# Kernel tuning notes

Hardware: AMD Instinct MI355X
Metric: run time of the kernel (lower is better)

Reference implementation:

```python
import jax, jax.numpy as jnp
import numpy as np

B, V, J, P = 1024, 5023, 5, 36
PARENTS = np.array([0, 0, 1, 1, 1], dtype=np.int64)  # FLAME kinematic chain


def setup_inputs() -> dict:
    key = jax.random.key(0)
    ks = jax.random.split(key, 8)
    return {
        "v_shaped_expressed": jax.random.normal(ks[0], (B, V, 3), jnp.float32) * 0.1,
        "global_pose_params_6d": jax.random.normal(ks[1], (B, 6), jnp.float32),
        "neck_pose_params_ax": jax.random.normal(ks[2], (B, 3), jnp.float32) * 0.1,
        "jaw_pose_params_ax": jax.random.normal(ks[3], (B, 3), jnp.float32) * 0.1,
        "eye_pose_params_ax": jax.random.normal(ks[4], (B, 6), jnp.float32) * 0.1,
        "J_transformed_rest": jax.random.normal(ks[5], (B, J, 3), jnp.float32) * 0.1,
        "lbs_weights": jax.nn.softmax(jax.random.normal(ks[6], (V, J), jnp.float32), axis=-1),
        "posedirs": jax.random.normal(ks[7], (V, P, 3), jnp.float32) * 0.01,
        "parents": jnp.asarray(PARENTS),
    }


def batch_rodrigues(rv, eps=1e-8):
    # rv: [B,3] axis-angle -> [B,3,3] rotation matrices
    angle = jnp.linalg.norm(rv + eps, axis=1, keepdims=True)  # [B,1]
    d = rv / angle
    cos = jnp.cos(angle)[:, :, None]
    sin = jnp.sin(angle)[:, :, None]
    rx, ry, rz = d[:, 0], d[:, 1], d[:, 2]
    z = jnp.zeros_like(rx)
    K = jnp.stack([z, -rz, ry, rz, z, -rx, -ry, rx, z], axis=1).reshape(-1, 3, 3)
    I = jnp.eye(3, dtype=rv.dtype)[None]
    return I + sin * K + (1.0 - cos) * (K @ K)


def rot6d_to_matrix(x):
    # Zhou et al. 6D rotation -> [B,3,3] (rows b1,b2,b3, as pytorch3d)
    a1, a2 = x[:, :3], x[:, 3:]
    b1 = a1 / jnp.linalg.norm(a1, axis=-1, keepdims=True)
    b2 = a2 - jnp.sum(b1 * a2, axis=-1, keepdims=True) * b1
    b2 = b2 / jnp.linalg.norm(b2, axis=-1, keepdims=True)
    b3 = jnp.cross(b1, b2)
    return jnp.stack([b1, b2, b3], axis=-2)


def make_T(R, t):
    # R [...,3,3], t [...,3] -> homogeneous [...,4,4]
    top = jnp.concatenate([R, t[..., None]], axis=-1)
    bot = jnp.broadcast_to(jnp.array([0.0, 0.0, 0.0, 1.0], R.dtype), top.shape[:-2] + (1, 4))
    return jnp.concatenate([top, bot], axis=-2)


def batch_rigid_transform(rot_mats, joints, parents):
    # rot_mats [B,J,3,3], joints [B,J,3]; parents: numpy int array (constant)
    rel = joints.at[:, 1:].add(-joints[:, parents[1:]])
    Tm = make_T(rot_mats, rel)  # [B,J,4,4]
    chain = [Tm[:, 0]]
    for i in range(1, parents.shape[0]):  # tiny fixed chain (J=5)
        chain.append(chain[int(parents[i])] @ Tm[:, i])
    tr = jnp.stack(chain, axis=1)  # [B,J,4,4]
    posed_joints = tr[:, :, :3, 3]
    R = tr[:, :, :3, :3]
    t = posed_joints - jnp.einsum('bjhw,bjw->bjh', R, joints)
    return posed_joints, make_T(R, t)


def reference(v_shaped_expressed, global_pose_params_6d, neck_pose_params_ax,
              jaw_pose_params_ax, eye_pose_params_ax, J_transformed_rest,
              lbs_weights, posedirs, parents):
    parents = np.asarray(parents)
    Rg = rot6d_to_matrix(global_pose_params_6d)
    Rn = batch_rodrigues(neck_pose_params_ax)
    Rj = batch_rodrigues(jaw_pose_params_ax)
    Rel = batch_rodrigues(eye_pose_params_ax[:, :3])
    Rer = batch_rodrigues(eye_pose_params_ax[:, 3:])
    rot_mats = jnp.stack([Rg, Rn, Rj, Rel, Rer], axis=1)  # [B,5,3,3]

    _, A = batch_rigid_transform(rot_mats, J_transformed_rest, parents)  # [B,5,4,4]

    # pose blendshapes from joints 1..4 (neck/jaw/eyes): [B, 36]
    b = rot_mats.shape[0]
    pose_feat = (rot_mats[:, 1:5] - jnp.eye(3, dtype=rot_mats.dtype)).reshape(b, -1)
    pose_bs = jnp.einsum('bp,vpc->bvc', pose_feat, posedirs)
    v = v_shaped_expressed + pose_bs  # [B,V,3]

    # linear blend skinning
    T = jnp.einsum('vj,bjhw->bvhw', lbs_weights, A)  # [B,V,4,4]
    v_h = jnp.concatenate([v, jnp.ones(v.shape[:2] + (1,), v.dtype)], axis=-1)
    v_posed = jnp.einsum('bvhw,bvw->bvh', T, v_h)[:, :, :3]
    return v_posed
```

## Files before the change

### kernel.cpp

```cpp
#include <hip/hip_runtime.h>
#include <math.h>

constexpr int Bn = 1024, Vn = 5023;
constexpr int NB = 32;
constexpr int PARAM_STRIDE = 96;


__device__ inline void rodrigues3(float rx, float ry, float rz, float R[9]) {
    const float eps = 1e-8f;
    float ax = rx + eps, ay = ry + eps, az = rz + eps;
    float ang = sqrtf(ax * ax + ay * ay + az * az);
    float inv = 1.0f / ang;
    float dx = rx * inv, dy = ry * inv, dz = rz * inv;
    float s = sinf(ang), c = cosf(ang), omc = 1.0f - c;
    float K[9] = {0.f, -dz, dy, dz, 0.f, -dx, -dy, dx, 0.f};
    float K2[9];
#pragma unroll
    for (int r = 0; r < 3; r++)
#pragma unroll
        for (int k = 0; k < 3; k++) {
            float acc = 0.f;
#pragma unroll
            for (int i = 0; i < 3; i++) acc += K[r * 3 + i] * K[i * 3 + k];
            K2[r * 3 + k] = acc;
        }
#pragma unroll
    for (int i = 0; i < 9; i++) R[i] = s * K[i] + omc * K2[i];
    R[0] += 1.f; R[4] += 1.f; R[8] += 1.f;
}

__device__ inline void rot6d(const float* x, float R[9]) {
    float a1x = x[0], a1y = x[1], a1z = x[2];
    float a2x = x[3], a2y = x[4], a2z = x[5];
    float n1 = sqrtf(a1x * a1x + a1y * a1y + a1z * a1z);
    float b1x = a1x / n1, b1y = a1y / n1, b1z = a1z / n1;
    float d = b1x * a2x + b1y * a2y + b1z * a2z;
    float tx = a2x - d * b1x, ty = a2y - d * b1y, tz = a2z - d * b1z;
    float n2 = sqrtf(tx * tx + ty * ty + tz * tz);
    float b2x = tx / n2, b2y = ty / n2, b2z = tz / n2;
    float b3x = b1y * b2z - b1z * b2y;
    float b3y = b1z * b2x - b1x * b2z;
    float b3z = b1x * b2y - b1y * b2x;
    R[0] = b1x; R[1] = b1y; R[2] = b1z;
    R[3] = b2x; R[4] = b2y; R[5] = b2z;
    R[6] = b3x; R[7] = b3y; R[8] = b3z;
}

__device__ inline void compose(const float* Rp, const float* tp,
                               const float* Ri, const float* ti,
                               float* Ro, float* to) {
#pragma unroll
    for (int r = 0; r < 3; r++) {
#pragma unroll
        for (int c = 0; c < 3; c++) {
            Ro[r * 3 + c] = Rp[r * 3 + 0] * Ri[0 * 3 + c] +
                            Rp[r * 3 + 1] * Ri[1 * 3 + c] +
                            Rp[r * 3 + 2] * Ri[2 * 3 + c];
        }
        to[r] = Rp[r * 3 + 0] * ti[0] + Rp[r * 3 + 1] * ti[1] +
                Rp[r * 3 + 2] * ti[2] + tp[r];
    }
}

__global__ void flame_params_kernel(const float* __restrict__ g6,
                                    const float* __restrict__ neck,
                                    const float* __restrict__ jaw,
                                    const float* __restrict__ eye,
                                    const float* __restrict__ jrest,
                                    float* __restrict__ params) {
    int b = blockIdx.x * blockDim.x + threadIdx.x;
    if (b >= Bn) return;

    float R[5][9];
    rot6d(g6 + b * 6, R[0]);
    rodrigues3(neck[b * 3 + 0], neck[b * 3 + 1], neck[b * 3 + 2], R[1]);
    rodrigues3(jaw[b * 3 + 0], jaw[b * 3 + 1], jaw[b * 3 + 2], R[2]);
    rodrigues3(eye[b * 6 + 0], eye[b * 6 + 1], eye[b * 6 + 2], R[3]);
    rodrigues3(eye[b * 6 + 3], eye[b * 6 + 4], eye[b * 6 + 5], R[4]);

    float j[5][3];
#pragma unroll
    for (int i = 0; i < 5; i++) {
        j[i][0] = jrest[b * 15 + i * 3 + 0];
        j[i][1] = jrest[b * 15 + i * 3 + 1];
        j[i][2] = jrest[b * 15 + i * 3 + 2];
    }
    float rel[5][3];
#pragma unroll
    for (int c = 0; c < 3; c++) {
        rel[0][c] = j[0][c];
        rel[1][c] = j[1][c] - j[0][c];
        rel[2][c] = j[2][c] - j[1][c];
        rel[3][c] = j[3][c] - j[1][c];
        rel[4][c] = j[4][c] - j[1][c];
    }

    float CR[5][9], CT[5][3];
#pragma unroll
    for (int i = 0; i < 9; i++) CR[0][i] = R[0][i];
#pragma unroll
    for (int c = 0; c < 3; c++) CT[0][c] = rel[0][c];
    compose(CR[0], CT[0], R[1], rel[1], CR[1], CT[1]);
    compose(CR[1], CT[1], R[2], rel[2], CR[2], CT[2]);
    compose(CR[1], CT[1], R[3], rel[3], CR[3], CT[3]);
    compose(CR[1], CT[1], R[4], rel[4], CR[4], CT[4]);

    float* P = params + b * PARAM_STRIDE;
#pragma unroll
    for (int jj = 0; jj < 4; jj++)
#pragma unroll
        for (int r = 0; r < 3; r++)
#pragma unroll
            for (int c = 0; c < 3; c++)
                P[jj * 9 + r * 3 + c] = R[jj + 1][r * 3 + c] - (r == c ? 1.f : 0.f);
#pragma unroll
    for (int i = 0; i < 5; i++) {
#pragma unroll
        for (int r = 0; r < 3; r++) {
            float t = CT[i][r] - (CR[i][r * 3 + 0] * j[i][0] +
                                  CR[i][r * 3 + 1] * j[i][1] +
                                  CR[i][r * 3 + 2] * j[i][2]);
            P[36 + i * 12 + r * 4 + 0] = CR[i][r * 3 + 0];
            P[36 + i * 12 + r * 4 + 1] = CR[i][r * 3 + 1];
            P[36 + i * 12 + r * 4 + 2] = CR[i][r * 3 + 2];
            P[36 + i * 12 + r * 4 + 3] = t;
        }
    }
}

__global__ __launch_bounds__(256) void flame_main_kernel(
    const float* __restrict__ vsh, const float* __restrict__ lbs,
    const float* __restrict__ pdirs, const float* __restrict__ params,
    float* __restrict__ out) {
    int v = blockIdx.x * 256 + threadIdx.x;
    bool valid = v < Vn;
    int vc = valid ? v : (Vn - 1);

    float pd[108];
#pragma unroll
    for (int i = 0; i < 27; i++) {
        float4 t = *reinterpret_cast<const float4*>(pdirs + (size_t)vc * 108 + i * 4);
        pd[i * 4 + 0] = t.x;
        pd[i * 4 + 1] = t.y;
        pd[i * 4 + 2] = t.z;
        pd[i * 4 + 3] = t.w;
    }
    float w[5];
#pragma unroll
    for (int jj = 0; jj < 5; jj++) w[jj] = lbs[(size_t)vc * 5 + jj];

    int b0 = blockIdx.y * NB;
    for (int bi = 0; bi < NB; bi++) {
        int b = b0 + bi;
        const float* __restrict__ P = params + b * PARAM_STRIDE;

        float ax = 0.f, ay = 0.f, az = 0.f;
#pragma unroll
        for (int p = 0; p < 36; p++) {
            float f = P[p];
            ax = fmaf(f, pd[p * 3 + 0], ax);
            ay = fmaf(f, pd[p * 3 + 1], ay);
            az = fmaf(f, pd[p * 3 + 2], az);
        }

        size_t base = ((size_t)b * Vn + vc) * 3;
        float x = vsh[base + 0] + ax;
        float y = vsh[base + 1] + ay;
        float z = vsh[base + 2] + az;

        float ox = 0.f, oy = 0.f, oz = 0.f;
#pragma unroll
        for (int jj = 0; jj < 5; jj++) {
            const float* Aj = P + 36 + jj * 12;
            float wj = w[jj];
            float rx = fmaf(Aj[0], x, fmaf(Aj[1], y, fmaf(Aj[2], z, Aj[3])));
            float ry = fmaf(Aj[4], x, fmaf(Aj[5], y, fmaf(Aj[6], z, Aj[7])));
            float rz = fmaf(Aj[8], x, fmaf(Aj[9], y, fmaf(Aj[10], z, Aj[11])));
            ox = fmaf(wj, rx, ox);
            oy = fmaf(wj, ry, oy);
            oz = fmaf(wj, rz, oz);
        }
        if (valid) {
            out[base + 0] = ox;
            out[base + 1] = oy;
            out[base + 2] = oz;
        }
    }
}

extern "C" void kernel_launch(void* const* d_in, const int* in_sizes, int n_in,
                              void* d_out, int out_size, void* d_ws, size_t ws_size,
                              hipStream_t stream) {
    const float* vsh   = (const float*)d_in[0];
    const float* g6    = (const float*)d_in[1];
    const float* neck  = (const float*)d_in[2];
    const float* jaw   = (const float*)d_in[3];
    const float* eye   = (const float*)d_in[4];
    const float* jrest = (const float*)d_in[5];
    const float* lbs   = (const float*)d_in[6];
    const float* pdirs = (const float*)d_in[7];
    float* out = (float*)d_out;
    float* params = (float*)d_ws;

    hipLaunchKernelGGL(flame_params_kernel, dim3((Bn + 255) / 256), dim3(256), 0,
                       stream, g6, neck, jaw, eye, jrest, params);

    dim3 grid((Vn + 255) / 256, Bn / NB);
    hipLaunchKernelGGL(flame_main_kernel, grid, dim3(256), 0, stream, vsh, lbs,
                       pdirs, params, out);
}
```

Baseline: 59.47 us.

## Stream posedirs in chunks and keep per-batch accumulators in registers

Instead of holding all 108 posedirs values per vertex in registers, the kernel loads them in 12-float chunks with a one-step software prefetch and applies each chunk to 8 batch accumulators. NB drops from 32 to 8, so the grid has more blocks along the batch axis and each block needs fewer registers, aiming at higher occupancy. The trade-off is that posedirs are reloaded by four times as many blocks, and param loads are spread through the loop.

```diff
diff --git a/kernel.cpp b/kernel.cpp
--- a/kernel.cpp
+++ b/kernel.cpp
@@ -2,7 +2,7 @@
 #include <math.h>
 
 constexpr int Bn = 1024, Vn = 5023;
-constexpr int NB = 32;
+constexpr int NB = 8;
 constexpr int PARAM_STRIDE = 96;
 
 
@@ -135,43 +135,59 @@
     int v = blockIdx.x * 256 + threadIdx.x;
     bool valid = v < Vn;
     int vc = valid ? v : (Vn - 1);
-
-    float pd[108];
-#pragma unroll
-    for (int i = 0; i < 27; i++) {
-        float4 t = *reinterpret_cast<const float4*>(pdirs + (size_t)vc * 108 + i * 4);
-        pd[i * 4 + 0] = t.x;
-        pd[i * 4 + 1] = t.y;
-        pd[i * 4 + 2] = t.z;
-        pd[i * 4 + 3] = t.w;
-    }
+    int b0 = blockIdx.y * NB;
+
+    float ax[NB], ay[NB], az[NB];
+#pragma unroll
+    for (int bi = 0; bi < NB; bi++) {
+        size_t base = ((size_t)(b0 + bi) * Vn + vc) * 3;
+        ax[bi] = vsh[base + 0];
+        ay[bi] = vsh[base + 1];
+        az[bi] = vsh[base + 2];
+    }
+
     float w[5];
 #pragma unroll
     for (int jj = 0; jj < 5; jj++) w[jj] = lbs[(size_t)vc * 5 + jj];
 
-    int b0 = blockIdx.y * NB;
+    const float* __restrict__ pv = pdirs + (size_t)vc * 108;
+    float4 c0 = *reinterpret_cast<const float4*>(pv + 0);
+    float4 c1 = *reinterpret_cast<const float4*>(pv + 4);
+    float4 c2 = *reinterpret_cast<const float4*>(pv + 8);
+
+#pragma unroll 1
+    for (int g = 0; g < 9; g++) {
+        float4 n0 = c0, n1 = c1, n2 = c2;
+        if (g < 8) {
+            n0 = *reinterpret_cast<const float4*>(pv + g * 12 + 12);
+            n1 = *reinterpret_cast<const float4*>(pv + g * 12 + 16);
+            n2 = *reinterpret_cast<const float4*>(pv + g * 12 + 20);
+        }
+        float pdv[12] = {c0.x, c0.y, c0.z, c0.w, c1.x, c1.y,
+                         c1.z, c1.w, c2.x, c2.y, c2.z, c2.w};
+#pragma unroll
+        for (int bi = 0; bi < NB; bi++) {
+            const float* __restrict__ P =
+                params + (b0 + bi) * PARAM_STRIDE + g * 4;
+#pragma unroll
+            for (int k = 0; k < 4; k++) {
+                float f = P[k];
+                ax[bi] = fmaf(f, pdv[k * 3 + 0], ax[bi]);
+                ay[bi] = fmaf(f, pdv[k * 3 + 1], ay[bi]);
+                az[bi] = fmaf(f, pdv[k * 3 + 2], az[bi]);
+            }
+        }
+        c0 = n0; c1 = n1; c2 = n2;
+    }
+
+#pragma unroll
     for (int bi = 0; bi < NB; bi++) {
-        int b = b0 + bi;
-        const float* __restrict__ P = params + b * PARAM_STRIDE;
-
-        float ax = 0.f, ay = 0.f, az = 0.f;
-#pragma unroll
-        for (int p = 0; p < 36; p++) {
-            float f = P[p];
-            ax = fmaf(f, pd[p * 3 + 0], ax);
-            ay = fmaf(f, pd[p * 3 + 1], ay);
-            az = fmaf(f, pd[p * 3 + 2], az);
-        }
-
-        size_t base = ((size_t)b * Vn + vc) * 3;
-        float x = vsh[base + 0] + ax;
-        float y = vsh[base + 1] + ay;
-        float z = vsh[base + 2] + az;
-
+        const float* __restrict__ A = params + (b0 + bi) * PARAM_STRIDE + 36;
+        float x = ax[bi], y = ay[bi], z = az[bi];
         float ox = 0.f, oy = 0.f, oz = 0.f;
 #pragma unroll
         for (int jj = 0; jj < 5; jj++) {
-            const float* Aj = P + 36 + jj * 12;
+            const float* Aj = A + jj * 12;
             float wj = w[jj];
             float rx = fmaf(Aj[0], x, fmaf(Aj[1], y, fmaf(Aj[2], z, Aj[3])));
             float ry = fmaf(Aj[4], x, fmaf(Aj[5], y, fmaf(Aj[6], z, Aj[7])));
@@ -181,6 +197,7 @@
             oz = fmaf(wj, rz, oz);
         }
         if (valid) {
+            size_t base = ((size_t)(b0 + bi) * Vn + vc) * 3;
             out[base + 0] = ox;
             out[base + 1] = oy;
             out[base + 2] = oz;
```

Result: slower. 61.26 us (+3.0%).

## Stage posedirs in LDS as packed bf16 and halve batch tile per block

Applied to the files above, without the earlier changes.

Posedirs for the block's 256 vertices are loaded with coalesced float4 reads, rounded to bf16, packed two per dword and stored in shared memory, so each thread no longer keeps 108 floats in registers. Per batch iteration the thread reads part of its row from LDS and keeps the rest in registers. Params are now read as float4, the loop is left un-unrolled, launch bounds ask for two blocks per SM, and NB drops to 16 to give more blocks. The aim is lower register pressure, better occupancy and coalesced loads, at the cost of bf16 rounding error in the pose blendshapes and about 60 KB of LDS per block.

```diff
diff --git a/kernel.cpp b/kernel.cpp
--- a/kernel.cpp
+++ b/kernel.cpp
@@ -2,8 +2,9 @@
 #include <math.h>
 
 constexpr int Bn = 1024, Vn = 5023;
-constexpr int NB = 32;
+constexpr int NB = 16;
 constexpr int PARAM_STRIDE = 96;
+constexpr int ROW_DW = 60;
 
 
 __device__ inline void rodrigues3(float rx, float ry, float rz, float R[9]) {
@@ -128,54 +129,109 @@
     }
 }
 
-__global__ __launch_bounds__(256) void flame_main_kernel(
+
+__device__ inline uint32_t pack_bf2(float a, float b) {
+    uint32_t ua = __float_as_uint(a);
+    uint32_t ub = __float_as_uint(b);
+    uint32_t ra = (ua + 0x7FFFu + ((ua >> 16) & 1u)) >> 16;
+    uint32_t rb = (ub + 0x7FFFu + ((ub >> 16) & 1u)) >> 16;
+    return (ra & 0xFFFFu) | (rb << 16);
+}
+
+#define GETD(i)                                                      \
+    (((i) & 3) == 0 ? C[(i) >> 2].x                                  \
+     : ((i) & 3) == 1 ? C[(i) >> 2].y                                \
+     : ((i) & 3) == 2 ? C[(i) >> 2].z : C[(i) >> 2].w)
+#define ACC(c) ((c) == 0 ? a0 : (c) == 1 ? a1 : a2)
+
+__global__ __launch_bounds__(256, 2) void flame_main_kernel(
     const float* __restrict__ vsh, const float* __restrict__ lbs,
     const float* __restrict__ pdirs, const float* __restrict__ params,
     float* __restrict__ out) {
-    int v = blockIdx.x * 256 + threadIdx.x;
+    int tid = threadIdx.x;
+    int v = blockIdx.x * 256 + tid;
     bool valid = v < Vn;
     int vc = valid ? v : (Vn - 1);
-
-    float pd[108];
-#pragma unroll
-    for (int i = 0; i < 27; i++) {
-        float4 t = *reinterpret_cast<const float4*>(pdirs + (size_t)vc * 108 + i * 4);
-        pd[i * 4 + 0] = t.x;
-        pd[i * 4 + 1] = t.y;
-        pd[i * 4 + 2] = t.z;
-        pd[i * 4 + 3] = t.w;
-    }
-    float w[5];
-#pragma unroll
-    for (int jj = 0; jj < 5; jj++) w[jj] = lbs[(size_t)vc * 5 + jj];
-
     int b0 = blockIdx.y * NB;
+
+    __shared__ uint32_t shd[256 * ROW_DW];
+
+    {
+        const size_t blk_base = (size_t)blockIdx.x * 256 * 108;
+        const size_t max_base = (size_t)Vn * 108 - 4;
+#pragma unroll
+        for (int c = 0; c < 27; c++) {
+            int q = c * 256 + tid;
+            size_t src = blk_base + (size_t)q * 4;
+            if (src > max_base) src = max_base;
+            float4 f = *reinterpret_cast<const float4*>(pdirs + src);
+            uint32_t d0 = pack_bf2(f.x, f.y);
+            uint32_t d1 = pack_bf2(f.z, f.w);
+            int p = q * 2;
+            int r = p / 54;
+            int k = p - r * 54;
+            shd[r * ROW_DW + k] = d0;
+            shd[r * ROW_DW + k + 1] = d1;
+        }
+    }
+    __syncthreads();
+
+    float wgt[5];
+#pragma unroll
+    for (int jj = 0; jj < 5; jj++) wgt[jj] = lbs[(size_t)vc * 5 + jj];
+
+    const uint4* __restrict__ my =
+        reinterpret_cast<const uint4*>(shd + tid * ROW_DW);
+
+    uint4 H0 = my[8], H1 = my[9], H2 = my[10], H3 = my[11], H4 = my[12],
+          H5 = my[13];
+
+#pragma unroll 1
     for (int bi = 0; bi < NB; bi++) {
         int b = b0 + bi;
-        const float* __restrict__ P = params + b * PARAM_STRIDE;
-
-        float ax = 0.f, ay = 0.f, az = 0.f;
-#pragma unroll
-        for (int p = 0; p < 36; p++) {
-            float f = P[p];
-            ax = fmaf(f, pd[p * 3 + 0], ax);
-            ay = fmaf(f, pd[p * 3 + 1], ay);
-            az = fmaf(f, pd[p * 3 + 2], az);
-        }
-
+        const float4* __restrict__ P4 =
+            reinterpret_cast<const float4*>(params + (size_t)b * PARAM_STRIDE);
         size_t base = ((size_t)b * Vn + vc) * 3;
-        float x = vsh[base + 0] + ax;
-        float y = vsh[base + 1] + ay;
-        float z = vsh[base + 2] + az;
+
+        float a0 = vsh[base + 0];
+        float a1 = vsh[base + 1];
+        float a2 = vsh[base + 2];
+
+        float fc[36];
+#pragma unroll
+        for (int g = 0; g < 9; g++) {
+            float4 f = P4[g];
+            fc[g * 4 + 0] = f.x;
+            fc[g * 4 + 1] = f.y;
+            fc[g * 4 + 2] = f.z;
+            fc[g * 4 + 3] = f.w;
+        }
+
+        uint4 C[14];
+#pragma unroll
+        for (int i = 0; i < 8; i++) C[i] = my[i];
+        C[8] = H0; C[9] = H1; C[10] = H2; C[11] = H3; C[12] = H4; C[13] = H5;
+
+#pragma unroll
+        for (int i = 0; i < 54; i++) {
+            uint32_t d = GETD(i);
+            float flo = __uint_as_float(d << 16);
+            float fhi = __uint_as_float(d & 0xFFFF0000u);
+            const int e0 = 2 * i, e1 = 2 * i + 1;
+            ACC(e0 % 3) = fmaf(fc[e0 / 3], flo, ACC(e0 % 3));
+            ACC(e1 % 3) = fmaf(fc[e1 / 3], fhi, ACC(e1 % 3));
+        }
 
         float ox = 0.f, oy = 0.f, oz = 0.f;
 #pragma unroll
         for (int jj = 0; jj < 5; jj++) {
-            const float* Aj = P + 36 + jj * 12;
-            float wj = w[jj];
-            float rx = fmaf(Aj[0], x, fmaf(Aj[1], y, fmaf(Aj[2], z, Aj[3])));
-            float ry = fmaf(Aj[4], x, fmaf(Aj[5], y, fmaf(Aj[6], z, Aj[7])));
-            float rz = fmaf(Aj[8], x, fmaf(Aj[9], y, fmaf(Aj[10], z, Aj[11])));
+            float4 r0 = P4[9 + jj * 3 + 0];
+            float4 r1 = P4[9 + jj * 3 + 1];
+            float4 r2 = P4[9 + jj * 3 + 2];
+            float wj = wgt[jj];
+            float rx = fmaf(r0.x, a0, fmaf(r0.y, a1, fmaf(r0.z, a2, r0.w)));
+            float ry = fmaf(r1.x, a0, fmaf(r1.y, a1, fmaf(r1.z, a2, r1.w)));
+            float rz = fmaf(r2.x, a0, fmaf(r2.y, a1, fmaf(r2.z, a2, r2.w)));
             ox = fmaf(wj, rx, ox);
             oy = fmaf(wj, ry, oy);
             oz = fmaf(wj, rz, oz);
```

Measured after the change: 70.13 us. 1.18x slower.

## Stage posedirs as fp16 in LDS and scalar-load per-batch params

Applied to the files above, without the earlier changes.

Each block now converts its 128 vertices' posedirs to packed fp16 in shared memory, instead of holding 108 floats per thread in registers. It splits the batch range between two half-blocks and reloads the posedirs into 27 packed registers per group of four batches. Per-batch pose features and joint transforms are fetched with inline-asm scalar loads into SGPRs. The goal is lower VGPR pressure, higher occupancy and better latency hiding for this bandwidth-bound loop, at the cost of fp16 rounding of the posedirs and reliance on fragile inline assembly. NB is halved and the grid is reshaped to match.

```diff
diff --git a/kernel.cpp b/kernel.cpp
--- a/kernel.cpp
+++ b/kernel.cpp
@@ -2,8 +2,13 @@
 #include <math.h>
 
 constexpr int Bn = 1024, Vn = 5023;
-constexpr int NB = 32;
+constexpr int NB = 16;
 constexpr int PARAM_STRIDE = 96;
+
+typedef int i32x16 __attribute__((ext_vector_type(16)));
+typedef int i32x8 __attribute__((ext_vector_type(8)));
+typedef int i32x4 __attribute__((ext_vector_type(4)));
+typedef __fp16 half2_t __attribute__((ext_vector_type(2)));
 
 
 __device__ inline void rodrigues3(float rx, float ry, float rz, float R[9]) {
@@ -128,62 +133,123 @@
     }
 }
 
-__global__ __launch_bounds__(256) void flame_main_kernel(
+
+#define FCV(k)                                                        \
+    __int_as_float((k) < 16 ? fc0[(k)]                                \
+                   : (k) < 32 ? fc1[(k) - 16] : fc2[(k) - 32])
+#define AFV(k)                                                        \
+    __int_as_float((k) < 16 ? A0[(k)]                                 \
+                   : (k) < 32 ? A1[(k) - 16]                          \
+                   : (k) < 48 ? A2[(k) - 32]                          \
+                   : (k) < 56 ? A3[(k) - 48] : A4[(k) - 56])
+#define ACCSEL(c) ((c) == 0 ? px : (c) == 1 ? py : pz)
+
+__global__ __launch_bounds__(256, 4) void flame_main_kernel(
     const float* __restrict__ vsh, const float* __restrict__ lbs,
     const float* __restrict__ pdirs, const float* __restrict__ params,
     float* __restrict__ out) {
-    int v = blockIdx.x * 256 + threadIdx.x;
-    bool valid = v < Vn;
-    int vc = valid ? v : (Vn - 1);
-
-    float pd[108];
-#pragma unroll
-    for (int i = 0; i < 27; i++) {
-        float4 t = *reinterpret_cast<const float4*>(pdirs + (size_t)vc * 108 + i * 4);
-        pd[i * 4 + 0] = t.x;
-        pd[i * 4 + 1] = t.y;
-        pd[i * 4 + 2] = t.z;
-        pd[i * 4 + 3] = t.w;
-    }
-    float w[5];
-#pragma unroll
-    for (int jj = 0; jj < 5; jj++) w[jj] = lbs[(size_t)vc * 5 + jj];
-
-    int b0 = blockIdx.y * NB;
-    for (int bi = 0; bi < NB; bi++) {
-        int b = b0 + bi;
-        const float* __restrict__ P = params + b * PARAM_STRIDE;
-
-        float ax = 0.f, ay = 0.f, az = 0.f;
-#pragma unroll
-        for (int p = 0; p < 36; p++) {
-            float f = P[p];
-            ax = fmaf(f, pd[p * 3 + 0], ax);
-            ay = fmaf(f, pd[p * 3 + 1], ay);
-            az = fmaf(f, pd[p * 3 + 2], az);
-        }
-
-        size_t base = ((size_t)b * Vn + vc) * 3;
-        float x = vsh[base + 0] + ax;
-        float y = vsh[base + 1] + ay;
-        float z = vsh[base + 2] + az;
-
-        float ox = 0.f, oy = 0.f, oz = 0.f;
-#pragma unroll
-        for (int jj = 0; jj < 5; jj++) {
-            const float* Aj = P + 36 + jj * 12;
-            float wj = w[jj];
-            float rx = fmaf(Aj[0], x, fmaf(Aj[1], y, fmaf(Aj[2], z, Aj[3])));
-            float ry = fmaf(Aj[4], x, fmaf(Aj[5], y, fmaf(Aj[6], z, Aj[7])));
-            float rz = fmaf(Aj[8], x, fmaf(Aj[9], y, fmaf(Aj[10], z, Aj[11])));
-            ox = fmaf(wj, rx, ox);
-            oy = fmaf(wj, ry, oy);
-            oz = fmaf(wj, rz, oz);
-        }
-        if (valid) {
-            out[base + 0] = ox;
-            out[base + 1] = oy;
-            out[base + 2] = oz;
+    const int tid = threadIdx.x;
+    const int vt = tid & 127;
+    const int bh = __builtin_amdgcn_readfirstlane(tid >> 7);
+    const int v = blockIdx.x * 128 + vt;
+    const bool valid = v < Vn;
+    const int vc = valid ? v : (Vn - 1);
+    const int b0 = blockIdx.y * NB + bh * (NB / 2);
+
+    __shared__ uint32_t shd[128 * 54];
+
+    {
+        const size_t g0 = (size_t)blockIdx.x * 128 * 108;
+        const size_t gmax = (size_t)Vn * 108 - 2;
+#pragma unroll
+        for (int i = 0; i < 27; i++) {
+            int p = i * 256 + tid;
+            size_t g = g0 + (size_t)p * 2;
+            if (g > gmax) g = gmax;
+            float2 f = *reinterpret_cast<const float2*>(pdirs + g);
+            half2_t h;
+            h.x = (__fp16)f.x;
+            h.y = (__fp16)f.y;
+            shd[p] = __builtin_bit_cast(uint32_t, h);
+        }
+    }
+    __syncthreads();
+
+    float wgt[5];
+#pragma unroll
+    for (int jj = 0; jj < 5; jj++) wgt[jj] = lbs[(size_t)vc * 5 + jj];
+
+    const uint2* __restrict__ my =
+        reinterpret_cast<const uint2*>(shd + vt * 54);
+
+#pragma unroll 1
+    for (int g2 = 0; g2 < 2; g2++) {
+        uint2 C[27];
+#pragma unroll
+        for (int i = 0; i < 27; i++) C[i] = my[i];
+
+#pragma unroll
+        for (int u = 0; u < 4; u++) {
+            const int b = b0 + g2 * 4 + u;
+            const float* P = params + (size_t)b * PARAM_STRIDE;
+            const size_t base = ((size_t)b * Vn + vc) * 3;
+
+            float a0 = vsh[base + 0];
+            float a1 = vsh[base + 1];
+            float a2 = vsh[base + 2];
+
+            i32x16 fc0, fc1;
+            i32x4 fc2;
+            asm volatile("s_load_dwordx16 %0, %1, 0x0" : "=s"(fc0) : "s"(P));
+            asm volatile("s_load_dwordx16 %0, %1, 0x40" : "=s"(fc1) : "s"(P));
+            asm volatile("s_load_dwordx4 %0, %1, 0x80" : "=s"(fc2) : "s"(P));
+            asm volatile("s_waitcnt lgkmcnt(0)" ::: "memory");
+            __builtin_amdgcn_sched_barrier(0);
+
+            float px = 0.f, py = 0.f, pz = 0.f;
+#pragma unroll
+            for (int i = 0; i < 54; i++) {
+                uint32_t dw = (i & 1) ? C[i >> 1].y : C[i >> 1].x;
+                half2_t h = __builtin_bit_cast(half2_t, dw);
+                float plo = (float)h.x;
+                float phi = (float)h.y;
+                const int e0 = 2 * i, e1 = 2 * i + 1;
+                ACCSEL(e0 % 3) = fmaf(FCV(e0 / 3), plo, ACCSEL(e0 % 3));
+                ACCSEL(e1 % 3) = fmaf(FCV(e1 / 3), phi, ACCSEL(e1 % 3));
+            }
+            float x = a0 + px, y = a1 + py, z = a2 + pz;
+
+            i32x16 A0, A1, A2;
+            i32x8 A3;
+            i32x4 A4;
+            asm volatile("s_load_dwordx16 %0, %1, 0x90" : "=s"(A0) : "s"(P));
+            asm volatile("s_load_dwordx16 %0, %1, 0xD0" : "=s"(A1) : "s"(P));
+            asm volatile("s_load_dwordx16 %0, %1, 0x110" : "=s"(A2) : "s"(P));
+            asm volatile("s_load_dwordx8 %0, %1, 0x150" : "=s"(A3) : "s"(P));
+            asm volatile("s_load_dwordx4 %0, %1, 0x170" : "=s"(A4) : "s"(P));
+            asm volatile("s_waitcnt lgkmcnt(0)" ::: "memory");
+            __builtin_amdgcn_sched_barrier(0);
+
+            float ox = 0.f, oy = 0.f, oz = 0.f;
+#pragma unroll
+            for (int jj = 0; jj < 5; jj++) {
+                const int o = jj * 12;
+                float wj = wgt[jj];
+                float rx = fmaf(AFV(o + 0), x,
+                           fmaf(AFV(o + 1), y, fmaf(AFV(o + 2), z, AFV(o + 3))));
+                float ry = fmaf(AFV(o + 4), x,
+                           fmaf(AFV(o + 5), y, fmaf(AFV(o + 6), z, AFV(o + 7))));
+                float rz = fmaf(AFV(o + 8), x,
+                           fmaf(AFV(o + 9), y, fmaf(AFV(o + 10), z, AFV(o + 11))));
+                ox = fmaf(wj, rx, ox);
+                oy = fmaf(wj, ry, oy);
+                oz = fmaf(wj, rz, oz);
+            }
+            if (valid) {
+                out[base + 0] = ox;
+                out[base + 1] = oy;
+                out[base + 2] = oz;
+            }
         }
     }
 }
@@ -205,7 +271,7 @@
     hipLaunchKernelGGL(flame_params_kernel, dim3((Bn + 255) / 256), dim3(256), 0,
                        stream, g6, neck, jaw, eye, jrest, params);
 
-    dim3 grid((Vn + 255) / 256, Bn / NB);
+    dim3 grid((Vn + 127) / 128, Bn / NB);
     hipLaunchKernelGGL(flame_main_kernel, grid, dim3(256), 0, stream, vsh, lbs,
                        pdirs, params, out);
 }
```

Result: slower. 100.2 us (+68.6%).
